# Kernel optimization log

Measured on AMD Instinct MI355X. Metric: run time of the kernel, lower is better.

The kernel has to match this reference:

```python
import jax, jax.numpy as jnp
import numpy as np

B, L, E, H = 32, 512, 1024, 1024


def setup_inputs() -> dict:
    key = jax.random.key(0)
    ks = jax.random.split(key, 12)
    s = 0.02
    return {
        "x": jax.random.normal(ks[0], (B, L, E), jnp.float32),
        "h0": jax.random.normal(ks[1], (B, L, H), jnp.float32),
        "c0": jax.random.normal(ks[2], (B, L, H), jnp.float32),
        "W_ioux": jax.random.normal(ks[3], (E, 3 * H), jnp.float32) * s,
        "W_iouh": jax.random.normal(ks[4], (2, H, 3 * H), jnp.float32) * s,
        "b_iouh": jax.random.normal(ks[5], (2, 3 * H), jnp.float32) * s,
        "W_fx": jax.random.normal(ks[6], (E, H), jnp.float32) * s,
        "W_fh": jax.random.normal(ks[7], (4, H, H), jnp.float32) * s,
        "b_fh": jax.random.normal(ks[8], (4, H), jnp.float32) * s,
        "tree_ids_d": jax.random.randint(ks[9], (B, L), 0, L, jnp.int32),
        "tree_ids_dr": jax.random.randint(ks[10], (B, L), 0, L, jnp.int32),
        "tree_ids_dl": jax.random.randint(ks[11], (B, L), 0, L, jnp.int32),
    }


def _scatter_add_rows(src, idx):
    # out[b, idx[b,l], :] += src[b, l, :]   (torch scatter_add_ on dim=1 with row-repeated index)
    b = jnp.arange(src.shape[0])[:, None]
    return jnp.zeros_like(src).at[b, idx].add(src)


def _gather_rows(src, idx):
    # out[b, l, :] = src[b, idx[b,l], :]    (torch gather on dim=1 with row-repeated index)
    return jnp.take_along_axis(src, idx[:, :, None], axis=1)


def _masked_scatter(dest, mask3, src):
    # torch masked_scatter_: True positions (flat order) filled with src elements in flat order
    mflat = mask3.reshape(-1)
    pos = jnp.cumsum(mflat.astype(jnp.int32)) - 1
    filled = jnp.take(src.reshape(-1), jnp.clip(pos, 0, src.size - 1))
    return jnp.where(mflat, filled, dest.reshape(-1)).reshape(dest.shape)


def reference(x, h0, c0, W_ioux, W_iouh, b_iouh, W_fx, W_fh, b_fh,
              tree_ids_d, tree_ids_dr, tree_ids_dl):
    Hh = h0.shape[-1]
    iou_x = x @ W_ioux                               # [B,L,3H]
    iou_hr = h0 @ W_iouh[0] + b_iouh[0]              # [B,L,3H]
    iou_hl = h0 @ W_iouh[1] + b_iouh[1]
    # original repeats index only to hidden_size -> only first H cols (i-gate) get scattered child states
    add = (_scatter_add_rows(iou_hr[..., :Hh], tree_ids_dr)
           + _scatter_add_rows(iou_hl[..., :Hh], tree_ids_dl))
    iou = iou_x.at[..., :Hh].add(add)
    i, o, u = jnp.split(iou, 3, axis=-1)
    i, o, u = jax.nn.sigmoid(i), jax.nn.sigmoid(o), jnp.tanh(u)

    fx = x @ W_fx                                    # [B,L,H]
    # fh[0],fh[1] both gathered at index_r; fh[2],fh[3] both at index_l -> fuse the GEMMs
    fr = h0 @ (W_fh[0] + W_fh[1]) + (b_fh[0] + b_fh[1])
    fl = h0 @ (W_fh[2] + W_fh[3]) + (b_fh[2] + b_fh[3])
    f = jax.nn.sigmoid(_gather_rows(fx, tree_ids_d)
                       + _gather_rows(fr, tree_ids_dr)
                       + _gather_rows(fl, tree_ids_dl))

    fc = f * c0
    c_new = i * u + _scatter_add_rows(fc, tree_ids_d)
    h_new = o * jnp.tanh(c_new)

    mask3 = jnp.broadcast_to((tree_ids_d != 0)[:, :, None], h_new.shape)
    h_out = _masked_scatter(h0, mask3, h_new)
    c_out = _masked_scatter(c0, mask3, c_new)
    return (h_out, c_out)
```

## Files before the change

kernel.cpp:

```cpp
#include <hip/hip_runtime.h>


#define ROWS 16384
#define HID  1024
#define KDIM 1024
#define NCOLS 4096
#define BM 256
#define BN 256

typedef __attribute__((ext_vector_type(4))) int            i32x4;
typedef __attribute__((ext_vector_type(4))) float          f32x4;
typedef __attribute__((ext_vector_type(4))) unsigned short u16x4;
typedef __attribute__((ext_vector_type(8))) unsigned short u16x8;

__device__ __forceinline__ unsigned short f2bf(float f) {
  unsigned u = __float_as_uint(f);
  unsigned r = 0x7FFFu + ((u >> 16) & 1u);
  return (unsigned short)((u + r) >> 16);
}
__device__ __forceinline__ float bf2f(unsigned short v) {
  return __uint_as_float(((unsigned)v) << 16);
}
__device__ __forceinline__ float sigmoidf_(float x) {
  return 1.0f / (1.0f + __expf(-x));
}
__device__ __forceinline__ void gload16(const void* g, void* l) {
  __builtin_amdgcn_global_load_lds(
      (const __attribute__((address_space(1))) void*)g,
      (__attribute__((address_space(3))) void*)l, 16, 0, 0);
}
__device__ __forceinline__ void mfma_bf16(f32x4& acc, i32x4 a, i32x4 b) {
  asm volatile("v_mfma_f32_16x16x32_bf16 %0, %1, %2, %0"
               : "+v"(acc) : "v"(a), "v"(b));
}


__global__ void pack_wx(const float* __restrict__ Wioux, const float* __restrict__ Wfx,
                        unsigned short* __restrict__ Wxt) {
  __shared__ float t[32][33];
  const int n0 = blockIdx.x * 32, k0 = blockIdx.y * 32;
  const int tx = threadIdx.x, ty = threadIdx.y;
  const int n = n0 + tx, k = k0 + ty;
  float v = (n < 3072) ? Wioux[(size_t)k * 3072 + n]
                       : Wfx[(size_t)k * 1024 + (n - 3072)];
  t[ty][tx] = v;
  __syncthreads();
  Wxt[(size_t)(n0 + ty) * KDIM + (k0 + tx)] = f2bf(t[tx][ty]);
}

__global__ void pack_wh(const float* __restrict__ Wiouh, const float* __restrict__ Wfh,
                        unsigned short* __restrict__ Wht) {
  __shared__ float t[32][33];
  const int n0 = blockIdx.x * 32, k0 = blockIdx.y * 32;
  const int tx = threadIdx.x, ty = threadIdx.y;
  const int n = n0 + tx, k = k0 + ty;
  float v;
  if (n < 1024)      v = Wiouh[(size_t)k * 3072 + n];
  else if (n < 2048) v = Wiouh[3145728u + (size_t)k * 3072 + (n - 1024)];
  else if (n < 3072) { const int c = n - 2048;
    v = Wfh[(size_t)k * 1024 + c] + Wfh[1048576u + (size_t)k * 1024 + c]; }
  else { const int c = n - 3072;
    v = Wfh[2097152u + (size_t)k * 1024 + c] + Wfh[3145728u + (size_t)k * 1024 + c]; }
  t[ty][tx] = v;
  __syncthreads();
  Wht[(size_t)(n0 + ty) * KDIM + (k0 + tx)] = f2bf(t[tx][ty]);
}

__global__ void pack_bias(const float* __restrict__ b_iouh, const float* __restrict__ b_fh,
                          float* __restrict__ bh) {
  const int n = blockIdx.x * 1024 + threadIdx.x;
  float v;
  if (n < 1024)      v = b_iouh[n];
  else if (n < 2048) v = b_iouh[3072 + (n - 1024)];
  else if (n < 3072) { const int c = n - 2048; v = b_fh[c] + b_fh[1024 + c]; }
  else { const int c = n - 3072; v = b_fh[2048 + c] + b_fh[3072 + c]; }
  bh[n] = v;
}

__global__ void convert_bf16(const float* __restrict__ x, const float* __restrict__ h0,
                             unsigned short* __restrict__ xb, unsigned short* __restrict__ hb) {
  const size_t i = ((size_t)blockIdx.x * 256 + threadIdx.x) * 4;
  const float4 a = *(const float4*)&x[i];
  const float4 b = *(const float4*)&h0[i];
  u16x4 av = { f2bf(a.x), f2bf(a.y), f2bf(a.z), f2bf(a.w) };
  u16x4 bv = { f2bf(b.x), f2bf(b.y), f2bf(b.z), f2bf(b.w) };
  *(u16x4*)&xb[i] = av;
  *(u16x4*)&hb[i] = bv;
}

__device__ __forceinline__ void stage8(const unsigned short* __restrict__ gp,
                                       unsigned short* __restrict__ lp,
                                       int rowbase, int gbase, int k0, int lane) {
  const int lrow = rowbase + (lane >> 3);
  const int sseg = (lane & 7) ^ ((lane >> 3) & 7);
  gload16(gp + (size_t)(gbase + lrow) * KDIM + k0 + sseg * 8,
          lp + ((size_t)rowbase << 6));
}

#define RD_A(dst, qm)                                                          \
  _Pragma("unroll")                                                            \
  for (int i = 0; i < 4; ++i) {                                                \
    const int row = wr * 128 + (qm) * 64 + i * 16 + m0;                        \
    _Pragma("unroll")                                                          \
    for (int s = 0; s < 2; ++s)                                                \
      dst[i][s] = *(const i32x4*)(Ab + row * 64 + (((kg + s * 4) ^ sw8) << 3)); \
  }

#define RD_B(dst, qn)                                                          \
  _Pragma("unroll")                                                            \
  for (int j = 0; j < 2; ++j) {                                                \
    const int col = wc * 64 + (qn) * 32 + j * 16 + m0;                         \
    _Pragma("unroll")                                                          \
    for (int s = 0; s < 2; ++s)                                                \
      dst[j][s] = *(const i32x4*)(Bb + col * 64 + (((kg + s * 4) ^ sw8) << 3)); \
  }

#define MM(afx, qmb, qnb)                                                      \
  __builtin_amdgcn_s_setprio(1);                                               \
  _Pragma("unroll")                                                            \
  for (int i = 0; i < 4; ++i)                                                  \
    _Pragma("unroll")                                                          \
    for (int j = 0; j < 2; ++j) {                                              \
      mfma_bf16(acc[(qmb) + i][(qnb) + j], afx[i][0], bfr[j][0]);              \
      mfma_bf16(acc[(qmb) + i][(qnb) + j], afx[i][1], bfr[j][1]);              \
    }                                                                          \
  __builtin_amdgcn_s_setprio(0);

__global__ __launch_bounds__(512, 2)
void gemm8(const unsigned short* __restrict__ xb, const unsigned short* __restrict__ hb,
           const unsigned short* __restrict__ Wxt, const unsigned short* __restrict__ Wht,
           unsigned short* __restrict__ gxb, unsigned short* __restrict__ ghb,
           const float* __restrict__ bhv) {
  __shared__ __align__(16) unsigned short S[2][2][256][64];

  const unsigned short* A;
  const unsigned short* Bt;
  unsigned short* Cp;
  const float* bias;
  if (blockIdx.z == 0) { A = xb; Bt = Wxt; Cp = gxb; bias = nullptr; }
  else                 { A = hb; Bt = Wht; Cp = ghb; bias = bhv; }

  int bx = blockIdx.x, by = blockIdx.y;
  const int ny = gridDim.y;
  if ((ny & 7) == 0) {
    const int n = blockIdx.x + 16 * blockIdx.y;
    const int xcd = n & 7, idx = n >> 3;
    const int ych = ny >> 3;
    bx = idx / ych;
    by = xcd * ych + (idx % ych);
  }
  const int bm = by * BM, bn = bx * BN;

  const int tid = threadIdx.x, w = tid >> 6, lane = tid & 63;
  const int wr = w >> 2, wc = w & 3;
  const int m0 = lane & 15, kg = lane >> 4, sw8 = m0 & 7;
  const int bq0 = ((w >> 1) << 6) + ((w & 1) << 4);

  f32x4 acc[8][4] = {};

  stage8(A,  &S[0][0][0][0], w * 8,        bm, 0, lane);
  stage8(A,  &S[0][0][0][0], 128 + w * 8,  bm, 0, lane);
  stage8(A,  &S[0][0][0][0], 64 + w * 8,   bm, 0, lane);
  stage8(A,  &S[0][0][0][0], 192 + w * 8,  bm, 0, lane);
  stage8(Bt, &S[0][1][0][0], bq0,          bn, 0, lane);
  stage8(Bt, &S[0][1][0][0], bq0 + 8,      bn, 0, lane);
  stage8(Bt, &S[0][1][0][0], bq0 + 32,     bn, 0, lane);
  stage8(Bt, &S[0][1][0][0], bq0 + 40,     bn, 0, lane);
  asm volatile("s_waitcnt vmcnt(0)" ::: "memory");
  __builtin_amdgcn_s_barrier();

  for (int t = 0; t < 16; ++t) {
    const int cur = t & 1, nxt = cur ^ 1;
    const unsigned short* Ab = &S[cur][0][0][0];
    const unsigned short* Bb = &S[cur][1][0][0];
    unsigned short* An = &S[nxt][0][0][0];
    unsigned short* Bn = &S[nxt][1][0][0];
    const int k1 = (t + 1) << 6;
    const bool st = (t < 15);
    i32x4 af0[4][2], af1[4][2], bfr[2][2];

    RD_A(af0, 0)
    RD_B(bfr, 0)
    if (st) { stage8(A, An, w * 8, bm, k1, lane);
              stage8(A, An, 128 + w * 8, bm, k1, lane);
              asm volatile("s_waitcnt vmcnt(4)" ::: "memory"); }
    else    { asm volatile("s_waitcnt vmcnt(2)" ::: "memory"); }
    __builtin_amdgcn_s_barrier();
    MM(af0, 0, 0)
    __builtin_amdgcn_s_barrier();

    RD_A(af1, 1)
    if (st) { stage8(Bt, Bn, bq0, bn, k1, lane);
              stage8(Bt, Bn, bq0 + 8, bn, k1, lane);
              asm volatile("s_waitcnt vmcnt(4)" ::: "memory"); }
    else    { asm volatile("s_waitcnt vmcnt(0)" ::: "memory"); }
    __builtin_amdgcn_s_barrier();
    MM(af1, 4, 0)
    __builtin_amdgcn_s_barrier();

    RD_B(bfr, 1)
    if (st) { stage8(A, An, 64 + w * 8, bm, k1, lane);
              stage8(A, An, 192 + w * 8, bm, k1, lane); }
    __builtin_amdgcn_s_barrier();
    MM(af1, 4, 2)
    __builtin_amdgcn_s_barrier();

    if (st) { stage8(Bt, Bn, bq0 + 32, bn, k1, lane);
              stage8(Bt, Bn, bq0 + 40, bn, k1, lane);
              asm volatile("s_waitcnt vmcnt(4)" ::: "memory"); }
    __builtin_amdgcn_s_barrier();
    MM(af0, 0, 2)
    __builtin_amdgcn_s_barrier();
  }

  __syncthreads();
  unsigned short* E = &S[0][0][0][0];
  const int rg = kg * 4;
#pragma unroll
  for (int mi = 0; mi < 8; ++mi) {
#pragma unroll
    for (int nj = 0; nj < 4; ++nj) {
      const int col = wc * 64 + nj * 16 + m0;
      const float bv = bias ? bias[bn + col] : 0.0f;
      const int rowb = wr * 128 + mi * 16 + rg;
#pragma unroll
      for (int r = 0; r < 4; ++r) {
        const int row = rowb + r;
        E[row * 256 + (col ^ (((row >> 2) & 3) << 4))] = f2bf(acc[mi][nj][r] + bv);
      }
    }
  }
  __syncthreads();
#pragma unroll
  for (int jj = 0; jj < 16; ++jj) {
    const int row = jj * 16 + (tid >> 5);
    const int c0 = (tid & 31) * 8;
    const int cs = c0 ^ (((row >> 2) & 3) << 4);
    const u16x8 v = *(const u16x8*)&E[row * 256 + cs];
    *(u16x8*)&Cp[(size_t)(bm + row) * NCOLS + bn + c0] = v;
  }
}

__global__ void scan_mask(const int* __restrict__ idd, int* __restrict__ sel,
                          int* __restrict__ mcount) {
  __shared__ int ps[1024];
  const int t = threadIdx.x;
  int loc[16];
  int cnt = 0;
#pragma unroll
  for (int i = 0; i < 16; ++i) {
    const int v = (idd[t * 16 + i] != 0) ? 1 : 0;
    loc[i] = v; cnt += v;
  }
  ps[t] = cnt;
  __syncthreads();
  for (int off = 1; off < 1024; off <<= 1) {
    const int add = (t >= off) ? ps[t - off] : 0;
    __syncthreads();
    ps[t] += add;
    __syncthreads();
  }
  int rank = (t == 0) ? 0 : ps[t - 1];
#pragma unroll
  for (int i = 0; i < 16; ++i)
    if (loc[i]) sel[rank++] = t * 16 + i;
  if (t == 1023) *mcount = ps[1023];
}

__global__ void build_csr(const int* __restrict__ idd, const int* __restrict__ idr,
                          const int* __restrict__ idl,
                          int* __restrict__ ofsD, int* __restrict__ ofsR, int* __restrict__ ofsL,
                          int* __restrict__ lstD, int* __restrict__ lstR, int* __restrict__ lstL) {
  __shared__ int sidx[512];
  __shared__ int scan[512];
  const int b = blockIdx.x, t = threadIdx.x;
  const int gb = b << 9;
  const int* const srcs[3] = { idd, idr, idl };
  int* const ofss[3] = { ofsD, ofsR, ofsL };
  int* const lsts[3] = { lstD, lstR, lstL };
  for (int a = 0; a < 3; ++a) {
    sidx[t] = srcs[a][gb + t];
    scan[t] = 0;
    __syncthreads();
    atomicAdd(&scan[sidx[t]], 1);
    __syncthreads();
    int v = scan[t];
    for (int off = 1; off < 512; off <<= 1) {
      const int add = (t >= off) ? scan[t - off] : 0;
      __syncthreads();
      scan[t] += add;
      __syncthreads();
    }
    const int start = scan[t] - v;
    ofss[a][b * 513 + t] = start;
    if (t == 511) ofss[a][b * 513 + 512] = scan[511];
    int pos = start;
    for (int l = 0; l < 512; ++l)
      if (sidx[l] == t) lsts[a][gb + (pos++)] = l;
    __syncthreads();
  }
}

__global__ __launch_bounds__(256)
void fused_final(const unsigned short* __restrict__ gxb, const unsigned short* __restrict__ ghb,
                 const float* __restrict__ h0, const float* __restrict__ c0,
                 const int* __restrict__ idd, const int* __restrict__ idr,
                 const int* __restrict__ idl,
                 const int* __restrict__ ofsR, const int* __restrict__ lstR,
                 const int* __restrict__ ofsL, const int* __restrict__ lstL,
                 const int* __restrict__ ofsD, const int* __restrict__ lstD,
                 const int* __restrict__ sel, const int* __restrict__ mcount,
                 float* __restrict__ hout, float* __restrict__ cout, int r0) {
  const int r = blockIdx.x;
  const int g = r0 + r;
  const int j = g & 511;
  const int bb = g >> 9;
  const int lbase = (r >> 9) << 9;
  const int ob = bb * 513;
  const int lb = bb << 9;
  const int c = threadIdx.x << 2;

  float a0 = 0.f, a1 = 0.f, a2 = 0.f, a3 = 0.f;
  for (int q = ofsR[ob + j], e = ofsR[ob + j + 1]; q < e; ++q) {
    const int l = lstR[lb + q];
    const u16x4 v = *(const u16x4*)&ghb[(size_t)(lbase + l) * NCOLS + c];
    a0 += bf2f(v[0]); a1 += bf2f(v[1]); a2 += bf2f(v[2]); a3 += bf2f(v[3]);
  }
  for (int q = ofsL[ob + j], e = ofsL[ob + j + 1]; q < e; ++q) {
    const int l = lstL[lb + q];
    const u16x4 v = *(const u16x4*)&ghb[(size_t)(lbase + l) * NCOLS + 1024 + c];
    a0 += bf2f(v[0]); a1 += bf2f(v[1]); a2 += bf2f(v[2]); a3 += bf2f(v[3]);
  }

  const u16x4 fx4 = *(const u16x4*)&gxb[(size_t)r * NCOLS + 3072 + c];
  const float fx0 = bf2f(fx4[0]), fx1 = bf2f(fx4[1]), fx2 = bf2f(fx4[2]), fx3 = bf2f(fx4[3]);
  float fc0 = 0.f, fc1 = 0.f, fc2 = 0.f, fc3 = 0.f;
  for (int q = ofsD[ob + j], e = ofsD[ob + j + 1]; q < e; ++q) {
    const int l = lstD[lb + q];
    const int jr = idr[lb + l], jl = idl[lb + l];
    const u16x4 rv = *(const u16x4*)&ghb[(size_t)(lbase + jr) * NCOLS + 2048 + c];
    const u16x4 lv = *(const u16x4*)&ghb[(size_t)(lbase + jl) * NCOLS + 3072 + c];
    const float4 cc = *(const float4*)&c0[(size_t)(lb + l) * HID + c];
    fc0 += sigmoidf_(fx0 + bf2f(rv[0]) + bf2f(lv[0])) * cc.x;
    fc1 += sigmoidf_(fx1 + bf2f(rv[1]) + bf2f(lv[1])) * cc.y;
    fc2 += sigmoidf_(fx2 + bf2f(rv[2]) + bf2f(lv[2])) * cc.z;
    fc3 += sigmoidf_(fx3 + bf2f(rv[3]) + bf2f(lv[3])) * cc.w;
  }

  const u16x4 vi = *(const u16x4*)&gxb[(size_t)r * NCOLS + c];
  const u16x4 vo = *(const u16x4*)&gxb[(size_t)r * NCOLS + 1024 + c];
  const u16x4 vu = *(const u16x4*)&gxb[(size_t)r * NCOLS + 2048 + c];
  float4 hn, cn;
  {
    const float ig = sigmoidf_(bf2f(vi[0]) + a0), og = sigmoidf_(bf2f(vo[0]));
    cn.x = ig * tanhf(bf2f(vu[0])) + fc0; hn.x = og * tanhf(cn.x);
  }
  {
    const float ig = sigmoidf_(bf2f(vi[1]) + a1), og = sigmoidf_(bf2f(vo[1]));
    cn.y = ig * tanhf(bf2f(vu[1])) + fc1; hn.y = og * tanhf(cn.y);
  }
  {
    const float ig = sigmoidf_(bf2f(vi[2]) + a2), og = sigmoidf_(bf2f(vo[2]));
    cn.z = ig * tanhf(bf2f(vu[2])) + fc2; hn.z = og * tanhf(cn.z);
  }
  {
    const float ig = sigmoidf_(bf2f(vi[3]) + a3), og = sigmoidf_(bf2f(vo[3]));
    cn.w = ig * tanhf(bf2f(vu[3])) + fc3; hn.w = og * tanhf(cn.w);
  }

  if (idd[g] == 0) {
    *(float4*)&hout[(size_t)g * HID + c] = *(const float4*)&h0[(size_t)g * HID + c];
    *(float4*)&cout[(size_t)g * HID + c] = *(const float4*)&c0[(size_t)g * HID + c];
  }
  const int m = *mcount;
  if (g < m) {
    const int o = sel[g];
    *(float4*)&hout[(size_t)o * HID + c] = hn;
    *(float4*)&cout[(size_t)o * HID + c] = cn;
  }
}

extern "C" void kernel_launch(void* const* d_in, const int* in_sizes, int n_in,
                              void* d_out, int out_size, void* d_ws, size_t ws_size,
                              hipStream_t stream) {
  const float* x      = (const float*)d_in[0];
  const float* h0     = (const float*)d_in[1];
  const float* c0     = (const float*)d_in[2];
  const float* W_ioux = (const float*)d_in[3];
  const float* W_iouh = (const float*)d_in[4];
  const float* b_iouh = (const float*)d_in[5];
  const float* W_fx   = (const float*)d_in[6];
  const float* W_fh   = (const float*)d_in[7];
  const float* b_fh   = (const float*)d_in[8];
  const int* idd      = (const int*)d_in[9];
  const int* idr      = (const int*)d_in[10];
  const int* idl      = (const int*)d_in[11];
  float* hout = (float*)d_out;
  float* cout = hout + (size_t)ROWS * HID;

  char* ws = (char*)d_ws;
  unsigned short* Wxt  = (unsigned short*)(ws);
  unsigned short* Wht  = (unsigned short*)(ws + 8388608u);
  float*          bh   = (float*)(ws + 16777216u);
  int*            sel  = (int*)(ws + 16793600u);
  int*            mcnt = (int*)(ws + 16859136u);
  int*            ofsD = (int*)(ws + 16859392u);
  int*            ofsR = (int*)(ws + 16925184u);
  int*            ofsL = (int*)(ws + 16990976u);
  int*            lstD = (int*)(ws + 17056768u);
  int*            lstR = (int*)(ws + 17122304u);
  int*            lstL = (int*)(ws + 17187840u);
  const size_t    base = 17253376u;

  int C = 32;
  while (C > 1 && base + 10485760ull * (size_t)C > ws_size) C >>= 1;
  const int R = 512 * C;

  char* p = ws + base;
  unsigned short* xb  = (unsigned short*)p;  p += 1048576ull * C;
  unsigned short* hb  = (unsigned short*)p;  p += 1048576ull * C;
  unsigned short* gxb = (unsigned short*)p;  p += 4194304ull * C;
  unsigned short* ghb = (unsigned short*)p;

  pack_wx<<<dim3(128, 32), dim3(32, 32), 0, stream>>>(W_ioux, W_fx, Wxt);
  pack_wh<<<dim3(128, 32), dim3(32, 32), 0, stream>>>(W_iouh, W_fh, Wht);
  pack_bias<<<4, 1024, 0, stream>>>(b_iouh, b_fh, bh);
  scan_mask<<<1, 1024, 0, stream>>>(idd, sel, mcnt);
  build_csr<<<32, 512, 0, stream>>>(idd, idr, idl, ofsD, ofsR, ofsL, lstD, lstR, lstL);

  for (int b0 = 0; b0 < 32; b0 += C) {
    const size_t r0 = (size_t)b0 * 512;
    convert_bf16<<<R, 256, 0, stream>>>(x + r0 * HID, h0 + r0 * HID, xb, hb);
    gemm8<<<dim3(NCOLS / BN, R / BM, 2), 512, 0, stream>>>(xb, hb, Wxt, Wht, gxb, ghb, bh);
    fused_final<<<R, 256, 0, stream>>>(gxb, ghb, h0, c0, idd, idr, idl,
                                       ofsR, lstR, ofsL, lstL, ofsD, lstD,
                                       sel, mcnt, hout, cout, (int)r0);
  }
}
```

Before: 527.0 us.

## Widen fused_final loads to 8 columns, pack D-edge indices, drop GEMM epilogue sync

The final elementwise kernel now handles 8 columns per thread, two rows per 256-thread block, with 16-byte bf16 loads. build_csr also writes an int4 list carrying (l, idr[l], idl[l]) per D-edge, so fused_final no longer makes dependent index lookups inside the f-gate gather loop. A __syncthreads before the GEMM epilogue writes to shared memory is removed, which risks a race if any wave is still reading the staging buffers when another starts writing the epilogue.

```diff
diff --git a/kernel.cpp b/kernel.cpp
--- a/kernel.cpp
+++ b/kernel.cpp
@@ -213,7 +213,6 @@
     __builtin_amdgcn_s_barrier();
   }
 
-  __syncthreads();
   unsigned short* E = &S[0][0][0][0];
   const int rg = kg * 4;
 #pragma unroll
@@ -270,7 +269,8 @@
 __global__ void build_csr(const int* __restrict__ idd, const int* __restrict__ idr,
                           const int* __restrict__ idl,
                           int* __restrict__ ofsD, int* __restrict__ ofsR, int* __restrict__ ofsL,
-                          int* __restrict__ lstD, int* __restrict__ lstR, int* __restrict__ lstL) {
+                          int* __restrict__ lstD, int* __restrict__ lstR, int* __restrict__ lstL,
+                          int4* __restrict__ lstDX) {
   __shared__ int sidx[512];
   __shared__ int scan[512];
   const int b = blockIdx.x, t = threadIdx.x;
@@ -299,84 +299,95 @@
       if (sidx[l] == t) lsts[a][gb + (pos++)] = l;
     __syncthreads();
   }
+  const int s0 = ofsD[b * 513 + t], s1 = ofsD[b * 513 + t + 1];
+  for (int q = s0; q < s1; ++q) {
+    const int l = lstD[gb + q];
+    int4 e;
+    e.x = l; e.y = idr[gb + l]; e.z = idl[gb + l]; e.w = 0;
+    lstDX[gb + q] = e;
+  }
 }
 
 __global__ __launch_bounds__(256)
 void fused_final(const unsigned short* __restrict__ gxb, const unsigned short* __restrict__ ghb,
                  const float* __restrict__ h0, const float* __restrict__ c0,
-                 const int* __restrict__ idd, const int* __restrict__ idr,
-                 const int* __restrict__ idl,
+                 const int* __restrict__ idd,
                  const int* __restrict__ ofsR, const int* __restrict__ lstR,
                  const int* __restrict__ ofsL, const int* __restrict__ lstL,
-                 const int* __restrict__ ofsD, const int* __restrict__ lstD,
+                 const int* __restrict__ ofsD, const int4* __restrict__ lstDX,
                  const int* __restrict__ sel, const int* __restrict__ mcount,
                  float* __restrict__ hout, float* __restrict__ cout, int r0) {
-  const int r = blockIdx.x;
+  const int sub = threadIdx.x >> 7;
+  const int ct  = threadIdx.x & 127;
+  const int r = blockIdx.x * 2 + sub;
   const int g = r0 + r;
   const int j = g & 511;
   const int bb = g >> 9;
   const int lbase = (r >> 9) << 9;
   const int ob = bb * 513;
   const int lb = bb << 9;
-  const int c = threadIdx.x << 2;
-
-  float a0 = 0.f, a1 = 0.f, a2 = 0.f, a3 = 0.f;
+  const int c = ct << 3;
+
+  float a[8] = {};
   for (int q = ofsR[ob + j], e = ofsR[ob + j + 1]; q < e; ++q) {
     const int l = lstR[lb + q];
-    const u16x4 v = *(const u16x4*)&ghb[(size_t)(lbase + l) * NCOLS + c];
-    a0 += bf2f(v[0]); a1 += bf2f(v[1]); a2 += bf2f(v[2]); a3 += bf2f(v[3]);
+    const u16x8 v = *(const u16x8*)&ghb[(size_t)(lbase + l) * NCOLS + c];
+#pragma unroll
+    for (int k = 0; k < 8; ++k) a[k] += bf2f(v[k]);
   }
   for (int q = ofsL[ob + j], e = ofsL[ob + j + 1]; q < e; ++q) {
     const int l = lstL[lb + q];
-    const u16x4 v = *(const u16x4*)&ghb[(size_t)(lbase + l) * NCOLS + 1024 + c];
-    a0 += bf2f(v[0]); a1 += bf2f(v[1]); a2 += bf2f(v[2]); a3 += bf2f(v[3]);
-  }
-
-  const u16x4 fx4 = *(const u16x4*)&gxb[(size_t)r * NCOLS + 3072 + c];
-  const float fx0 = bf2f(fx4[0]), fx1 = bf2f(fx4[1]), fx2 = bf2f(fx4[2]), fx3 = bf2f(fx4[3]);
-  float fc0 = 0.f, fc1 = 0.f, fc2 = 0.f, fc3 = 0.f;
+    const u16x8 v = *(const u16x8*)&ghb[(size_t)(lbase + l) * NCOLS + 1024 + c];
+#pragma unroll
+    for (int k = 0; k < 8; ++k) a[k] += bf2f(v[k]);
+  }
+
+  const u16x8 fx8 = *(const u16x8*)&gxb[(size_t)r * NCOLS + 3072 + c];
+  float fx[8];
+#pragma unroll
+  for (int k = 0; k < 8; ++k) fx[k] = bf2f(fx8[k]);
+  float fc[8] = {};
   for (int q = ofsD[ob + j], e = ofsD[ob + j + 1]; q < e; ++q) {
-    const int l = lstD[lb + q];
-    const int jr = idr[lb + l], jl = idl[lb + l];
-    const u16x4 rv = *(const u16x4*)&ghb[(size_t)(lbase + jr) * NCOLS + 2048 + c];
-    const u16x4 lv = *(const u16x4*)&ghb[(size_t)(lbase + jl) * NCOLS + 3072 + c];
-    const float4 cc = *(const float4*)&c0[(size_t)(lb + l) * HID + c];
-    fc0 += sigmoidf_(fx0 + bf2f(rv[0]) + bf2f(lv[0])) * cc.x;
-    fc1 += sigmoidf_(fx1 + bf2f(rv[1]) + bf2f(lv[1])) * cc.y;
-    fc2 += sigmoidf_(fx2 + bf2f(rv[2]) + bf2f(lv[2])) * cc.z;
-    fc3 += sigmoidf_(fx3 + bf2f(rv[3]) + bf2f(lv[3])) * cc.w;
-  }
-
-  const u16x4 vi = *(const u16x4*)&gxb[(size_t)r * NCOLS + c];
-  const u16x4 vo = *(const u16x4*)&gxb[(size_t)r * NCOLS + 1024 + c];
-  const u16x4 vu = *(const u16x4*)&gxb[(size_t)r * NCOLS + 2048 + c];
-  float4 hn, cn;
-  {
-    const float ig = sigmoidf_(bf2f(vi[0]) + a0), og = sigmoidf_(bf2f(vo[0]));
-    cn.x = ig * tanhf(bf2f(vu[0])) + fc0; hn.x = og * tanhf(cn.x);
-  }
-  {
-    const float ig = sigmoidf_(bf2f(vi[1]) + a1), og = sigmoidf_(bf2f(vo[1]));
-    cn.y = ig * tanhf(bf2f(vu[1])) + fc1; hn.y = og * tanhf(cn.y);
-  }
-  {
-    const float ig = sigmoidf_(bf2f(vi[2]) + a2), og = sigmoidf_(bf2f(vo[2]));
-    cn.z = ig * tanhf(bf2f(vu[2])) + fc2; hn.z = og * tanhf(cn.z);
-  }
-  {
-    const float ig = sigmoidf_(bf2f(vi[3]) + a3), og = sigmoidf_(bf2f(vo[3]));
-    cn.w = ig * tanhf(bf2f(vu[3])) + fc3; hn.w = og * tanhf(cn.w);
+    const int4 dx = lstDX[lb + q];
+    const int l = dx.x, jr = dx.y, jl = dx.z;
+    const u16x8 rv = *(const u16x8*)&ghb[(size_t)(lbase + jr) * NCOLS + 2048 + c];
+    const u16x8 lv = *(const u16x8*)&ghb[(size_t)(lbase + jl) * NCOLS + 3072 + c];
+    const float4 c0a = *(const float4*)&c0[(size_t)(lb + l) * HID + c];
+    const float4 c0b = *(const float4*)&c0[(size_t)(lb + l) * HID + c + 4];
+    const float cc[8] = { c0a.x, c0a.y, c0a.z, c0a.w, c0b.x, c0b.y, c0b.z, c0b.w };
+#pragma unroll
+    for (int k = 0; k < 8; ++k)
+      fc[k] += sigmoidf_(fx[k] + bf2f(rv[k]) + bf2f(lv[k])) * cc[k];
+  }
+
+  const u16x8 vi = *(const u16x8*)&gxb[(size_t)r * NCOLS + c];
+  const u16x8 vo = *(const u16x8*)&gxb[(size_t)r * NCOLS + 1024 + c];
+  const u16x8 vu = *(const u16x8*)&gxb[(size_t)r * NCOLS + 2048 + c];
+  float hn[8], cn[8];
+#pragma unroll
+  for (int k = 0; k < 8; ++k) {
+    const float ig = sigmoidf_(bf2f(vi[k]) + a[k]);
+    const float og = sigmoidf_(bf2f(vo[k]));
+    cn[k] = ig * tanhf(bf2f(vu[k])) + fc[k];
+    hn[k] = og * tanhf(cn[k]);
   }
 
   if (idd[g] == 0) {
-    *(float4*)&hout[(size_t)g * HID + c] = *(const float4*)&h0[(size_t)g * HID + c];
-    *(float4*)&cout[(size_t)g * HID + c] = *(const float4*)&c0[(size_t)g * HID + c];
+#pragma unroll
+    for (int h = 0; h < 2; ++h) {
+      *(float4*)&hout[(size_t)g * HID + c + h * 4] =
+          *(const float4*)&h0[(size_t)g * HID + c + h * 4];
+      *(float4*)&cout[(size_t)g * HID + c + h * 4] =
+          *(const float4*)&c0[(size_t)g * HID + c + h * 4];
+    }
   }
   const int m = *mcount;
   if (g < m) {
     const int o = sel[g];
-    *(float4*)&hout[(size_t)o * HID + c] = hn;
-    *(float4*)&cout[(size_t)o * HID + c] = cn;
+    *(float4*)&hout[(size_t)o * HID + c]     = make_float4(hn[0], hn[1], hn[2], hn[3]);
+    *(float4*)&hout[(size_t)o * HID + c + 4] = make_float4(hn[4], hn[5], hn[6], hn[7]);
+    *(float4*)&cout[(size_t)o * HID + c]     = make_float4(cn[0], cn[1], cn[2], cn[3]);
+    *(float4*)&cout[(size_t)o * HID + c + 4] = make_float4(cn[4], cn[5], cn[6], cn[7]);
   }
 }
 
@@ -410,7 +421,8 @@
   int*            lstD = (int*)(ws + 17056768u);
   int*            lstR = (int*)(ws + 17122304u);
   int*            lstL = (int*)(ws + 17187840u);
-  const size_t    base = 17253376u;
+  int4*           lstDX= (int4*)(ws + 17253376u);
+  const size_t    base = 17515520u;
 
   int C = 32;
   while (C > 1 && base + 10485760ull * (size_t)C > ws_size) C >>= 1;
@@ -426,14 +438,15 @@
   pack_wh<<<dim3(128, 32), dim3(32, 32), 0, stream>>>(W_iouh, W_fh, Wht);
   pack_bias<<<4, 1024, 0, stream>>>(b_iouh, b_fh, bh);
   scan_mask<<<1, 1024, 0, stream>>>(idd, sel, mcnt);
-  build_csr<<<32, 512, 0, stream>>>(idd, idr, idl, ofsD, ofsR, ofsL, lstD, lstR, lstL);
+  build_csr<<<32, 512, 0, stream>>>(idd, idr, idl, ofsD, ofsR, ofsL,
+                                    lstD, lstR, lstL, lstDX);
 
   for (int b0 = 0; b0 < 32; b0 += C) {
     const size_t r0 = (size_t)b0 * 512;
     convert_bf16<<<R, 256, 0, stream>>>(x + r0 * HID, h0 + r0 * HID, xb, hb);
     gemm8<<<dim3(NCOLS / BN, R / BM, 2), 512, 0, stream>>>(xb, hb, Wxt, Wht, gxb, ghb, bh);
-    fused_final<<<R, 256, 0, stream>>>(gxb, ghb, h0, c0, idd, idr, idl,
-                                       ofsR, lstR, ofsL, lstL, ofsD, lstD,
-                                       sel, mcnt, hout, cout, (int)r0);
-  }
-}
+    fused_final<<<R / 2, 256, 0, stream>>>(gxb, ghb, h0, c0, idd,
+                                           ofsR, lstR, ofsL, lstL, ofsD, lstDX,
+                                           sel, mcnt, hout, cout, (int)r0);
+  }
+}
```

New measurement: 548.8 us. 4.1% more time.
